# Optimization experiments

Measured on AMD Instinct MI355X. Metric: run time of the kernel, lower is better.

## Reference

```python
import jax, jax.numpy as jnp
import numpy as np
import math

B, T, C = 2, 8192, 1024
H = 16
HD = C // H  # 64
WIN = 256    # local_window_size


def _rope_tables(T, hd):
    inv_freq = 1.0 / (10000.0 ** (np.arange(0, hd, 2, dtype=np.float32) / hd))
    t = np.arange(T, dtype=np.float32)
    freqs = np.outer(t, inv_freq)                      # [T, hd/2]
    emb = np.concatenate([freqs, freqs], axis=-1)      # [T, hd]
    return jnp.asarray(np.cos(emb))[None, None], jnp.asarray(np.sin(emb))[None, None]


def setup_inputs() -> dict:
    key = jax.random.key(0)
    ks = jax.random.split(key, 10)
    x = jax.random.normal(ks[0], (B, T, C), dtype=jnp.float32)
    # padding_mask: bool [B,T]; per the source, True positions end up masked out of attention
    padding_mask = jax.random.randint(ks[1], (B, T), 0, 2).astype(bool)
    cos, sin = _rope_tables(T, HD)                     # [1,1,T,HD]
    s = 1.0 / math.sqrt(C)
    Wq = jax.random.normal(ks[2], (C, C), dtype=jnp.float32) * s
    bq = jnp.zeros((C,), dtype=jnp.float32)
    Wk = jax.random.normal(ks[3], (C, C), dtype=jnp.float32) * s
    bk = jnp.zeros((C,), dtype=jnp.float32)
    Wv = jax.random.normal(ks[4], (C, C), dtype=jnp.float32) * s
    bv = jnp.zeros((C,), dtype=jnp.float32)
    Wo = jax.random.normal(ks[5], (C, C), dtype=jnp.float32) * s
    bo = jnp.zeros((C,), dtype=jnp.float32)
    return {"x": x, "padding_mask": padding_mask, "cos": cos, "sin": sin,
            "Wq": Wq, "bq": bq, "Wk": Wk, "bk": bk, "Wv": Wv, "bv": bv,
            "Wo": Wo, "bo": bo}


def _rotate_half(t):
    h = t.shape[-1] // 2
    return jnp.concatenate([-t[..., h:], t[..., :h]], axis=-1)


def reference(x, padding_mask, cos, sin, Wq, bq, Wk, bk, Wv, bv, Wo, bo):
    Bx, Tx, Cx = x.shape
    Wn = WIN
    pad_end = (Wn - Tx % Wn) % Wn            # static python int
    Tp = Tx + pad_end
    nW = Tp // Wn
    half = Wn // 2
    hd = cos.shape[-1]

    cos_t = jnp.broadcast_to(cos[0, 0][None], (Bx, Tx, hd))
    sin_t = jnp.broadcast_to(sin[0, 0][None], (Bx, Tx, hd))
    if pad_end > 0:
        x = jnp.pad(x, ((0, 0), (0, pad_end), (0, 0)))
        padding_mask = jnp.pad(padding_mask, ((0, 0), (0, pad_end)))
        cos_t = jnp.pad(cos_t, ((0, 0), (0, pad_end), (0, 0)))
        sin_t = jnp.pad(sin_t, ((0, 0), (0, pad_end), (0, 0)))

    # non-overlapping query windows: [B*nW, W, C]
    q_win = x.reshape(Bx * nW, Wn, Cx)
    cos_q = cos_t.reshape(Bx * nW, Wn, hd)[:, None]   # [Bw,1,W,hd]
    sin_q = sin_t.reshape(Bx * nW, Wn, hd)[:, None]

    # overlapping key/value windows of size 2W, stride W
    x_ctx = jnp.pad(x, ((0, 0), (half, half), (0, 0)))
    cos_ctx = jnp.pad(cos_t, ((0, 0), (half, half), (0, 0)))
    sin_ctx = jnp.pad(sin_t, ((0, 0), (half, half), (0, 0)))
    pk = jnp.pad(padding_mask, ((0, 0), (half, half)))  # pad value False
    idx = jnp.arange(nW)[:, None] * Wn + jnp.arange(2 * Wn)[None, :]  # [nW, 2W]
    k_win = x_ctx[:, idx].reshape(Bx * nW, 2 * Wn, Cx)
    cos_k = cos_ctx[:, idx].reshape(Bx * nW, 2 * Wn, hd)[:, None]
    sin_k = sin_ctx[:, idx].reshape(Bx * nW, 2 * Wn, hd)[:, None]
    pk = pk[:, idx].reshape(Bx * nW, 2 * Wn)

    # attn_mask: True = attend (SDPA bool-mask convention)
    attn_mask = ~pk
    all_attend = jnp.all(attn_mask, axis=-1)
    attn_mask = attn_mask.at[:, 0].set(jnp.where(all_attend, False, attn_mask[:, 0]))

    Bw = Bx * nW
    q = (q_win @ Wq.T + bq).reshape(Bw, Wn, H, HD).transpose(0, 2, 1, 3)        # [Bw,H,W,hd]
    k = (k_win @ Wk.T + bk).reshape(Bw, 2 * Wn, H, HD).transpose(0, 2, 1, 3)    # [Bw,H,2W,hd]
    v = (k_win @ Wv.T + bv).reshape(Bw, 2 * Wn, H, HD).transpose(0, 2, 1, 3)

    q = q * cos_q + _rotate_half(q) * sin_q
    k = k * cos_k + _rotate_half(k) * sin_k

    scale = 1.0 / math.sqrt(HD)
    scores = jnp.einsum('bhqd,bhkd->bhqk', q, k) * scale                        # [Bw,H,W,2W]
    scores = jnp.where(attn_mask[:, None, None, :], scores, jnp.finfo(scores.dtype).min)
    attn = jax.nn.softmax(scores, axis=-1)
    out = jnp.einsum('bhqk,bhkd->bhqd', attn, v)
    out = out.transpose(0, 2, 1, 3).reshape(Bw, Wn, Cx)
    out = out @ Wo.T + bo
    out = out.reshape(Bx, nW * Wn, Cx)[:, :Tx]
    return out
```

## Files before the change

kernel.cpp:

```cpp
#include <hip/hip_runtime.h>
#include <hip/hip_bf16.h>
#include <stdint.h>

#define T_SEQ 8192
#define B_SZ 2
#define CDIM 1024
#define NH 16
#define HDIM 64
#define NW 32

typedef unsigned short ushort_t;
typedef __attribute__((ext_vector_type(8))) short short8;
typedef __attribute__((ext_vector_type(8))) unsigned short us8;
typedef __attribute__((ext_vector_type(4))) unsigned short us4;
typedef __attribute__((ext_vector_type(4))) float f32x4;

__device__ __forceinline__ unsigned short f2bf(float f) {
  union { float f; unsigned int u; } c; c.f = f;
  return (unsigned short)((c.u + 0x7FFFu + ((c.u >> 16) & 1u)) >> 16);
}
__device__ __forceinline__ unsigned pk2(float a, float b) {
  unsigned r;
  asm("v_cvt_pk_bf16_f32 %0, %1, %2" : "=v"(r) : "v"(a), "v"(b));
  return r;
}
__device__ __forceinline__ void gld16(void* lds, const void* g) {
  __builtin_amdgcn_global_load_lds(
      (const __attribute__((address_space(1))) void*)g,
      (__attribute__((address_space(3))) void*)lds, 16, 0, 0);
}

__global__ __launch_bounds__(256) void cvt_f32_bf16(const float* __restrict__ src,
                                                    ushort_t* __restrict__ dst, int n4)
{
  int i = blockIdx.x * 256 + threadIdx.x;
  if (i < n4) {
    float4 v = ((const float4*)src)[i];
    ushort4 o;
    o.x = f2bf(v.x); o.y = f2bf(v.y); o.z = f2bf(v.z); o.w = f2bf(v.w);
    ((ushort4*)dst)[i] = o;
  }
}

__global__ __launch_bounds__(256) void cvt_w4(const float* __restrict__ w0,
                                              const float* __restrict__ w1,
                                              const float* __restrict__ w2,
                                              const float* __restrict__ w3,
                                              ushort_t* __restrict__ dst)
{
  const float* srcs[4] = {w0, w1, w2, w3};
  const float* s = srcs[blockIdx.y];
  ushort_t* d = dst + (size_t)blockIdx.y * CDIM * CDIM;
  int i = blockIdx.x * 256 + threadIdx.x;
  float4 v = ((const float4*)s)[i];
  ushort4 o;
  o.x = f2bf(v.x); o.y = f2bf(v.y); o.z = f2bf(v.z); o.w = f2bf(v.w);
  ((ushort4*)d)[i] = o;
}

__device__ __forceinline__ void gemm256_core(const ushort_t* __restrict__ A,
                                             const ushort_t* __restrict__ W,
                                             ushort_t* SH,
                                             int m0, int n0, int t, f32x4 acc[8][4])
{
  const int lane = t & 63;
  const int wv = t >> 6;
  const int wr = wv >> 2;
  const int wc = wv & 3;
  const int fr = lane & 15;
  const int quad = lane >> 4;

  ushort_t* As = SH;
  ushort_t* Bs = SH + 32768;

  const int sr8 = lane >> 3;
  const int scb = ((lane & 7) ^ sr8) * 8;
  const int srowb = wv * 8 + sr8;
  const ushort_t* Ag = A + (size_t)(m0 + srowb) * CDIM + scb;
  const ushort_t* Wg = W + (size_t)(n0 + srowb) * CDIM + scb;
  ushort_t* lA = As + srowb * 64 + (lane & 7) * 8;
  ushort_t* lB = Bs + srowb * 64 + (lane & 7) * 8;

#pragma unroll
  for (int p = 0; p < 4; p++) {
    gld16(lA + p * 4096, Ag + (size_t)p * 64 * CDIM);
    gld16(lB + p * 4096, Wg + (size_t)p * 64 * CDIM);
  }
  __syncthreads();

  for (int kt = 0; kt < CDIM / 64; ++kt) {
    const int cur = kt & 1;
    if (kt + 1 < CDIM / 64) {
      const ushort_t* Agn = Ag + (kt + 1) * 64;
      const ushort_t* Wgn = Wg + (kt + 1) * 64;
      ushort_t* nA = lA + (cur ^ 1) * 16384;
      ushort_t* nB = lB + (cur ^ 1) * 16384;
#pragma unroll
      for (int p = 0; p < 4; p++) {
        gld16(nA + p * 4096, Agn + (size_t)p * 64 * CDIM);
        gld16(nB + p * 4096, Wgn + (size_t)p * 64 * CDIM);
      }
    }
    const ushort_t* Ac = As + cur * 16384;
    const ushort_t* Bc = Bs + cur * 16384;
    short8 b[4][2];
#pragma unroll
    for (int j = 0; j < 4; j++)
#pragma unroll
      for (int ks = 0; ks < 2; ks++)
        b[j][ks] = *(const short8*)&Bc[(wc * 64 + j * 16 + fr) * 64 +
                                       (((ks * 4 + quad) ^ (fr & 7)) * 8)];
    __builtin_amdgcn_s_setprio(1);
#pragma unroll
    for (int i = 0; i < 8; i++) {
      const int ra = (wr * 128 + i * 16 + fr) * 64;
      short8 a0 = *(const short8*)&Ac[ra + ((quad ^ (fr & 7)) * 8)];
      short8 a1 = *(const short8*)&Ac[ra + (((4 + quad) ^ (fr & 7)) * 8)];
#pragma unroll
      for (int j = 0; j < 4; j++)
        acc[i][j] = __builtin_amdgcn_mfma_f32_16x16x32_bf16(a0, b[j][0], acc[i][j], 0, 0, 0);
#pragma unroll
      for (int j = 0; j < 4; j++)
        acc[i][j] = __builtin_amdgcn_mfma_f32_16x16x32_bf16(a1, b[j][1], acc[i][j], 0, 0, 0);
    }
    __builtin_amdgcn_s_setprio(0);
    __syncthreads();
  }
}

__device__ __forceinline__ void xcd_swz(int& bx, int& by) {
  int gx = gridDim.x, nwg = gx * gridDim.y;
  int lid = bx + gx * by;
  int cpx = nwg >> 3;
  int swz = (lid & 7) * cpx + (lid >> 3);
  bx = swz % gx;
  by = swz / gx;
}

__global__ __launch_bounds__(512, 1) void gemm_qkv(const ushort_t* __restrict__ A,
                                                   const ushort_t* __restrict__ Wcat,
                                                   const float* __restrict__ bq,
                                                   const float* __restrict__ bk,
                                                   const float* __restrict__ bv,
                                                   ushort_t* __restrict__ Qb,
                                                   ushort_t* __restrict__ Kb,
                                                   ushort_t* __restrict__ Vtb,
                                                   const float* __restrict__ cosT,
                                                   const float* __restrict__ sinT)
{
  extern __shared__ ushort_t SH[];

  const int t = threadIdx.x;
  const int lane = t & 63;
  const int wv = t >> 6;
  const int wr = wv >> 2;
  const int wc = wv & 3;
  const int fr = lane & 15;
  const int quad = lane >> 4;
  int bx = blockIdx.x, by = blockIdx.y;
  xcd_swz(bx, by);
  const int m0 = by * 256;
  const int n0 = bx * 256;
  const int sec = bx >> 2;
  const int nsec0 = (bx & 3) * 256;
  const float* bias = (sec == 0) ? bq : (sec == 1) ? bk : bv;

  f32x4 acc[8][4];
#pragma unroll
  for (int i = 0; i < 8; i++)
#pragma unroll
    for (int j = 0; j < 4; j++) acc[i][j] = (f32x4){0.f, 0.f, 0.f, 0.f};

  gemm256_core(A, Wcat, SH, m0, n0, t, acc);

  if (sec < 2) {
    ushort_t* OutQK = sec ? Kb : Qb;
#pragma unroll
    for (int half = 0; half < 2; ++half) {
      if (wr == half) {
#pragma unroll
        for (int jp = 0; jp < 2; jp++) {
          int d = jp * 16 + fr;
          int cl = wc * 64 + jp * 16 + fr;
          float bl = bias[nsec0 + cl];
          float bh = bias[nsec0 + cl + 32];
#pragma unroll
          for (int i = 0; i < 8; i++) {
            int rloc = i * 16 + quad * 4;
#pragma unroll
            for (int r = 0; r < 4; r++) {
              int m = m0 + half * 128 + rloc + r;
              int tt = m & (T_SEQ - 1);
              float c = cosT[tt * HDIM + d];
              float sn = sinT[tt * HDIM + d];
              float lo = acc[i][jp][r] + bl;
              float hi = acc[i][jp + 2][r] + bh;
              SH[(rloc + r) * 264 + cl] = f2bf(lo * c - hi * sn);
              SH[(rloc + r) * 264 + cl + 32] = f2bf(hi * c + lo * sn);
            }
          }
        }
      }
      __syncthreads();
      const int rr0 = t >> 5;
      const int c8 = (t & 31) * 8;
      size_t gbase = (size_t)(m0 + half * 128) * CDIM + nsec0 + c8;
#pragma unroll
      for (int pp = 0; pp < 8; pp++) {
        int rr = pp * 16 + rr0;
        *(us8*)&OutQK[gbase + (size_t)rr * CDIM] = *(const us8*)&SH[rr * 264 + c8];
      }
      __syncthreads();
    }
  } else {
#pragma unroll
    for (int j = 0; j < 4; j++) {
      int ch = nsec0 + wc * 64 + j * 16 + fr;
      float bvv = bias[ch];
#pragma unroll
      for (int i = 0; i < 8; i++) {
        int m = m0 + wr * 128 + i * 16 + quad * 4;
        int bb = m >> 13;
        int tq = m & (T_SEQ - 1);
        us4 pk;
#pragma unroll
        for (int r = 0; r < 4; r++) pk[r] = f2bf(acc[i][j][r] + bvv);
        *(us4*)&Vtb[((size_t)bb * CDIM + ch) * T_SEQ + tq] = pk;
      }
    }
  }
}

__global__ __launch_bounds__(512, 1) void gemm_out(const ushort_t* __restrict__ A,
                                                   const ushort_t* __restrict__ W,
                                                   const float* __restrict__ bias,
                                                   float* __restrict__ Out)
{
  extern __shared__ ushort_t SH[];

  const int t = threadIdx.x;
  const int lane = t & 63;
  const int wv = t >> 6;
  const int wr = wv >> 2;
  const int wc = wv & 3;
  const int fr = lane & 15;
  const int quad = lane >> 4;
  int bx = blockIdx.x, by = blockIdx.y;
  xcd_swz(bx, by);
  const int m0 = by * 256;
  const int n0 = bx * 256;

  f32x4 acc[8][4];
#pragma unroll
  for (int i = 0; i < 8; i++)
#pragma unroll
    for (int j = 0; j < 4; j++) acc[i][j] = (f32x4){0.f, 0.f, 0.f, 0.f};

  gemm256_core(A, W, SH, m0, n0, t, acc);

#pragma unroll
  for (int j = 0; j < 4; j++) {
    int n = n0 + wc * 64 + j * 16 + fr;
    float bvv = bias[n];
#pragma unroll
    for (int i = 0; i < 8; i++) {
      int m = m0 + wr * 128 + i * 16 + quad * 4;
#pragma unroll
      for (int r = 0; r < 4; r++)
        Out[(size_t)(m + r) * CDIM + n] = acc[i][j][r] + bvv;
    }
  }
}

__global__ __launch_bounds__(256, 4) void attn_kernel(const ushort_t* __restrict__ Q,
                                                      const ushort_t* __restrict__ Kg,
                                                      const ushort_t* __restrict__ Vt,
                                                      const int* __restrict__ mask,
                                                      ushort_t* __restrict__ AO)
{
  __shared__ ushort_t Ks[64 * 72];
  __shared__ ushort_t Vts[64 * 72];
  __shared__ unsigned int PsW[4 * 32 * 32];
  __shared__ float attf[512];

  const int t = threadIdx.x;
  const int lane = t & 63;
  const int wv = t >> 6;
  const int h = blockIdx.x;
  const int w = blockIdx.y >> 1;
  const int qh = blockIdx.y & 1;
  const int b = blockIdx.z;
  const int fr = lane & 15;
  const int quad = lane >> 4;

  {
    int p0 = w * 256 + t - 128;
    bool a0 = (p0 < 0 || p0 >= T_SEQ) ? true : (mask[b * T_SEQ + p0] == 0);
    int p1 = p0 + 256;
    bool a1 = (p1 < 0 || p1 >= T_SEQ) ? true : (mask[b * T_SEQ + p1] == 0);
    int all1 = __syncthreads_and((int)(a0 && a1));
    attf[t] = a0 ? 0.f : -1.0e38f;
    attf[t + 256] = a1 ? 0.f : -1.0e38f;
    if (all1 && t == 0) attf[0] = -1.0e38f;
  }

  short8 qf[2][2];
  {
    const ushort_t* qp = Q + ((size_t)b * T_SEQ + w * 256 + qh * 128 + wv * 32 + fr) * CDIM
                           + h * HDIM + quad * 8;
#pragma unroll
    for (int mt = 0; mt < 2; mt++)
#pragma unroll
      for (int ks = 0; ks < 2; ks++)
        qf[mt][ks] = *(const short8*)&qp[(size_t)mt * 16 * CDIM + ks * 32];
  }

  const int srow = t >> 3;
  const int sc8 = (t & 7) * 8;
  const ushort_t* kgb = Kg + (size_t)b * T_SEQ * CDIM + h * HDIM + sc8;
  const ushort_t* vt_base = Vt + ((size_t)b * CDIM + h * HDIM) * T_SEQ;
  const float SCL = 0.18033688011112042f;

  unsigned int* pw = &PsW[wv * 1024];
  const int swz = (fr & 7) << 2;
  const int rbase = quad << 2;

  float m_run[2], l_run[2];
  f32x4 o[2][4];
#pragma unroll
  for (int mt = 0; mt < 2; mt++) { m_run[mt] = -3.0e38f; l_run[mt] = 0.f; }
#pragma unroll
  for (int mt = 0; mt < 2; mt++)
#pragma unroll
    for (int nt = 0; nt < 4; nt++) o[mt][nt] = (f32x4){0.f, 0.f, 0.f, 0.f};

  for (int kc = 0; kc < 8; kc++) {
    __syncthreads();
    {
#pragma unroll
      for (int p = 0; p < 2; p++) {
        int jj = p * 32 + srow;
        int pos = w * 256 + kc * 64 + jj - 128;
        us8 kval = (us8)(0);
        if (pos >= 0 && pos < T_SEQ) kval = *(const us8*)&kgb[(size_t)pos * CDIM];
        *(us8*)&Ks[jj * 72 + sc8] = kval;
      }
      int pos0 = w * 256 + kc * 64 - 128 + sc8;
      bool inr = (pos0 >= 0) && (pos0 < T_SEQ);
#pragma unroll
      for (int p = 0; p < 2; p++) {
        int d = p * 32 + srow;
        us8 vv = (us8)(0);
        if (inr) vv = *(const us8*)&vt_base[(size_t)d * T_SEQ + pos0];
        *(us8*)&Vts[d * 72 + sc8] = vv;
      }
    }
    __syncthreads();

    short8 kf[4][2];
#pragma unroll
    for (int nt = 0; nt < 4; nt++)
#pragma unroll
      for (int ks = 0; ks < 2; ks++)
        kf[nt][ks] = *(const short8*)&Ks[(nt * 16 + fr) * 72 + ks * 32 + quad * 8];

    f32x4 st[2][4];
    __builtin_amdgcn_s_setprio(1);
#pragma unroll
    for (int mt = 0; mt < 2; mt++)
#pragma unroll
      for (int nt = 0; nt < 4; nt++) {
        f32x4 a = (f32x4){0.f, 0.f, 0.f, 0.f};
        a = __builtin_amdgcn_mfma_f32_16x16x32_bf16(kf[nt][0], qf[mt][0], a, 0, 0, 0);
        a = __builtin_amdgcn_mfma_f32_16x16x32_bf16(kf[nt][1], qf[mt][1], a, 0, 0, 0);
        st[mt][nt] = a;
      }
    __builtin_amdgcn_s_setprio(0);

    f32x4 kb[4];
#pragma unroll
    for (int nt = 0; nt < 4; nt++)
      kb[nt] = *(const f32x4*)&attf[kc * 64 + nt * 16 + quad * 4];
#pragma unroll
    for (int mt = 0; mt < 2; mt++)
#pragma unroll
      for (int nt = 0; nt < 4; nt++)
#pragma unroll
        for (int r = 0; r < 4; r++)
          st[mt][nt][r] = __builtin_fmaf(st[mt][nt][r], SCL, kb[nt][r]);

#pragma unroll
    for (int mt = 0; mt < 2; mt++) {
      float t0 = fmaxf(fmaxf(st[mt][0][0], st[mt][0][1]), fmaxf(st[mt][0][2], st[mt][0][3]));
      float t1 = fmaxf(fmaxf(st[mt][1][0], st[mt][1][1]), fmaxf(st[mt][1][2], st[mt][1][3]));
      float t2 = fmaxf(fmaxf(st[mt][2][0], st[mt][2][1]), fmaxf(st[mt][2][2], st[mt][2][3]));
      float t3 = fmaxf(fmaxf(st[mt][3][0], st[mt][3][1]), fmaxf(st[mt][3][2], st[mt][3][3]));
      float mx = fmaxf(fmaxf(t0, t1), fmaxf(t2, t3));
      mx = fmaxf(mx, __shfl_xor(mx, 16, 64));
      mx = fmaxf(mx, __shfl_xor(mx, 32, 64));
      if (!__all(mx <= m_run[mt] + 8.f)) {
        float mnew = fmaxf(m_run[mt], mx);
        float alpha = __builtin_amdgcn_exp2f(m_run[mt] - mnew);
        m_run[mt] = mnew;
        l_run[mt] *= alpha;
        float af[4];
#pragma unroll
        for (int r = 0; r < 4; r++) af[r] = __shfl(alpha, rbase + r, 64);
#pragma unroll
        for (int nt = 0; nt < 4; nt++)
#pragma unroll
          for (int r = 0; r < 4; r++) o[mt][nt][r] *= af[r];
      }
      float rs = 0.f;
#pragma unroll
      for (int nt = 0; nt < 4; nt++)
#pragma unroll
        for (int r = 0; r < 4; r++) {
          float p = __builtin_amdgcn_exp2f(st[mt][nt][r] - m_run[mt]);
          st[mt][nt][r] = p;
          rs += p;
        }
      rs += __shfl_xor(rs, 16, 64);
      rs += __shfl_xor(rs, 32, 64);
      l_run[mt] += rs;

      unsigned int* pr = pw + ((mt * 16 + fr) << 5);
#pragma unroll
      for (int nt = 0; nt < 4; nt++)
#pragma unroll
        for (int hh = 0; hh < 2; hh++)
          pr[(((nt << 3) + (quad << 1) + hh)) ^ swz] =
              pk2(st[mt][nt][2 * hh], st[mt][nt][2 * hh + 1]);
    }

    short8 vf[4][2];
#pragma unroll
    for (int nt = 0; nt < 4; nt++)
#pragma unroll
      for (int ks = 0; ks < 2; ks++)
        vf[nt][ks] = *(const short8*)&Vts[(nt * 16 + fr) * 72 + ks * 32 + quad * 8];

    __builtin_amdgcn_s_setprio(1);
#pragma unroll
    for (int mt = 0; mt < 2; mt++) {
      const unsigned int* pr = pw + ((mt * 16 + fr) << 5);
      short8 pf[2];
#pragma unroll
      for (int ks = 0; ks < 2; ks++)
        pf[ks] = *(const short8*)&pr[((ks << 4) + (quad << 2)) ^ swz];
#pragma unroll
      for (int nt = 0; nt < 4; nt++) {
        o[mt][nt] = __builtin_amdgcn_mfma_f32_16x16x32_bf16(pf[0], vf[nt][0], o[mt][nt], 0, 0, 0);
        o[mt][nt] = __builtin_amdgcn_mfma_f32_16x16x32_bf16(pf[1], vf[nt][1], o[mt][nt], 0, 0, 0);
      }
    }
    __builtin_amdgcn_s_setprio(0);
  }

  size_t obase = ((size_t)b * T_SEQ + w * 256 + qh * 128 + wv * 32) * CDIM + h * HDIM;
#pragma unroll
  for (int mt = 0; mt < 2; mt++)
#pragma unroll
    for (int r = 0; r < 4; r++) {
      float lv = __shfl(l_run[mt], rbase + r, 64);
      float iv = 1.0f / fmaxf(lv, 1e-30f);
      int row = mt * 16 + quad * 4 + r;
#pragma unroll
      for (int nt = 0; nt < 4; nt++)
        AO[obase + (size_t)row * CDIM + nt * 16 + fr] = f2bf(o[mt][nt][r] * iv);
    }
}

extern "C" void kernel_launch(void* const* d_in, const int* in_sizes, int n_in,
                              void* d_out, int out_size, void* d_ws, size_t ws_size,
                              hipStream_t stream)
{
  const float* x    = (const float*)d_in[0];
  const int*   pm   = (const int*)d_in[1];
  const float* cosT = (const float*)d_in[2];
  const float* sinT = (const float*)d_in[3];
  const float* Wq   = (const float*)d_in[4];
  const float* bq   = (const float*)d_in[5];
  const float* Wk   = (const float*)d_in[6];
  const float* bk   = (const float*)d_in[7];
  const float* Wv   = (const float*)d_in[8];
  const float* bv   = (const float*)d_in[9];
  const float* Wo   = (const float*)d_in[10];
  const float* bo   = (const float*)d_in[11];
  float* out = (float*)d_out;

  static bool attr_done = false;
  if (!attr_done) {
    hipFuncSetAttribute(reinterpret_cast<const void*>(gemm_qkv),
                        hipFuncAttributeMaxDynamicSharedMemorySize, 131072);
    hipFuncSetAttribute(reinterpret_cast<const void*>(gemm_out),
                        hipFuncAttributeMaxDynamicSharedMemorySize, 131072);
    attr_done = true;
  }

  const size_t NTOK = (size_t)B_SZ * T_SEQ;
  const size_t NELT = NTOK * CDIM;
  ushort_t* Kb  = (ushort_t*)d_out;
  ushort_t* xbf = (ushort_t*)d_out + NELT;
  char* ws = (char*)d_ws;
  ushort_t* Wbf = (ushort_t*)ws;
  ushort_t* Qb  = (ushort_t*)(ws + 4 * (size_t)CDIM * CDIM * 2);
  ushort_t* Vtb = Qb + NELT;
  ushort_t* AO  = Qb;

  cvt_f32_bf16<<<(int)(NELT / 4 / 256), 256, 0, stream>>>(x, xbf, (int)(NELT / 4));
  cvt_w4<<<dim3(CDIM * CDIM / 4 / 256, 4), 256, 0, stream>>>(Wq, Wk, Wv, Wo, Wbf);

  gemm_qkv<<<dim3(12, (int)(NTOK / 256)), 512, 131072, stream>>>(
      xbf, Wbf, bq, bk, bv, Qb, Kb, Vtb, cosT, sinT);

  attn_kernel<<<dim3(NH, NW * 2, B_SZ), 256, 0, stream>>>(Qb, Kb, Vtb, pm, AO);

  gemm_out<<<dim3(4, (int)(NTOK / 256)), 512, 131072, stream>>>(
      AO, Wbf + 3 * (size_t)CDIM * CDIM, bo, out);
}
```

Baseline: 406.8 us.

## Halve GEMM K-tile to 32 and allow two workgroups per CU

The shared GEMM core now stages 32-wide K slices instead of 64, using a 4-way XOR swizzle, which halves LDS per workgroup (64KB double-buffered). Launch bounds change from 1 to 2 blocks per CU so two 512-thread workgroups can co-reside and hide latency. The cost is twice as many K iterations with a barrier each, and a tighter register budget (acc[8][4] per thread) that may cause spills.

```diff
diff --git a/kernel.cpp b/kernel.cpp
--- a/kernel.cpp
+++ b/kernel.cpp
@@ -71,57 +71,49 @@
   const int quad = lane >> 4;
 
   ushort_t* As = SH;
-  ushort_t* Bs = SH + 32768;
-
-  const int sr8 = lane >> 3;
-  const int scb = ((lane & 7) ^ sr8) * 8;
-  const int srowb = wv * 8 + sr8;
-  const ushort_t* Ag = A + (size_t)(m0 + srowb) * CDIM + scb;
-  const ushort_t* Wg = W + (size_t)(n0 + srowb) * CDIM + scb;
-  ushort_t* lA = As + srowb * 64 + (lane & 7) * 8;
-  ushort_t* lB = Bs + srowb * 64 + (lane & 7) * 8;
-
-#pragma unroll
-  for (int p = 0; p < 4; p++) {
-    gld16(lA + p * 4096, Ag + (size_t)p * 64 * CDIM);
-    gld16(lB + p * 4096, Wg + (size_t)p * 64 * CDIM);
+  ushort_t* Bs = SH + 16384;
+
+  const int r0 = wv * 16 + (lane >> 2);
+  const int scb = ((lane & 3) ^ (r0 & 3)) * 8;
+  const ushort_t* Ag = A + (size_t)(m0 + r0) * CDIM + scb;
+  const ushort_t* Wg = W + (size_t)(n0 + r0) * CDIM + scb;
+  ushort_t* lA = As + r0 * 32 + (lane & 3) * 8;
+  ushort_t* lB = Bs + r0 * 32 + (lane & 3) * 8;
+
+#pragma unroll
+  for (int p = 0; p < 2; p++) {
+    gld16(lA + p * 4096, Ag + (size_t)p * 128 * CDIM);
+    gld16(lB + p * 4096, Wg + (size_t)p * 128 * CDIM);
   }
   __syncthreads();
 
-  for (int kt = 0; kt < CDIM / 64; ++kt) {
+  const int rblk = (quad ^ (fr & 3)) * 8;
+
+  for (int kt = 0; kt < CDIM / 32; ++kt) {
     const int cur = kt & 1;
-    if (kt + 1 < CDIM / 64) {
-      const ushort_t* Agn = Ag + (kt + 1) * 64;
-      const ushort_t* Wgn = Wg + (kt + 1) * 64;
-      ushort_t* nA = lA + (cur ^ 1) * 16384;
-      ushort_t* nB = lB + (cur ^ 1) * 16384;
-#pragma unroll
-      for (int p = 0; p < 4; p++) {
-        gld16(nA + p * 4096, Agn + (size_t)p * 64 * CDIM);
-        gld16(nB + p * 4096, Wgn + (size_t)p * 64 * CDIM);
-      }
-    }
-    const ushort_t* Ac = As + cur * 16384;
-    const ushort_t* Bc = Bs + cur * 16384;
-    short8 b[4][2];
+    if (kt + 1 < CDIM / 32) {
+      const int kc = (kt + 1) * 32;
+      ushort_t* nA = lA + (cur ^ 1) * 8192;
+      ushort_t* nB = lB + (cur ^ 1) * 8192;
+#pragma unroll
+      for (int p = 0; p < 2; p++) {
+        gld16(nA + p * 4096, Ag + (size_t)p * 128 * CDIM + kc);
+        gld16(nB + p * 4096, Wg + (size_t)p * 128 * CDIM + kc);
+      }
+    }
+    const ushort_t* Ac = As + cur * 8192;
+    const ushort_t* Bc = Bs + cur * 8192;
+    short8 b[4];
 #pragma unroll
     for (int j = 0; j < 4; j++)
-#pragma unroll
-      for (int ks = 0; ks < 2; ks++)
-        b[j][ks] = *(const short8*)&Bc[(wc * 64 + j * 16 + fr) * 64 +
-                                       (((ks * 4 + quad) ^ (fr & 7)) * 8)];
+      b[j] = *(const short8*)&Bc[(wc * 64 + j * 16 + fr) * 32 + rblk];
     __builtin_amdgcn_s_setprio(1);
 #pragma unroll
     for (int i = 0; i < 8; i++) {
-      const int ra = (wr * 128 + i * 16 + fr) * 64;
-      short8 a0 = *(const short8*)&Ac[ra + ((quad ^ (fr & 7)) * 8)];
-      short8 a1 = *(const short8*)&Ac[ra + (((4 + quad) ^ (fr & 7)) * 8)];
+      short8 a = *(const short8*)&Ac[(wr * 128 + i * 16 + fr) * 32 + rblk];
 #pragma unroll
       for (int j = 0; j < 4; j++)
-        acc[i][j] = __builtin_amdgcn_mfma_f32_16x16x32_bf16(a0, b[j][0], acc[i][j], 0, 0, 0);
-#pragma unroll
-      for (int j = 0; j < 4; j++)
-        acc[i][j] = __builtin_amdgcn_mfma_f32_16x16x32_bf16(a1, b[j][1], acc[i][j], 0, 0, 0);
+        acc[i][j] = __builtin_amdgcn_mfma_f32_16x16x32_bf16(a, b[j], acc[i][j], 0, 0, 0);
     }
     __builtin_amdgcn_s_setprio(0);
     __syncthreads();
@@ -137,7 +129,7 @@
   by = swz / gx;
 }
 
-__global__ __launch_bounds__(512, 1) void gemm_qkv(const ushort_t* __restrict__ A,
+__global__ __launch_bounds__(512, 2) void gemm_qkv(const ushort_t* __restrict__ A,
                                                    const ushort_t* __restrict__ Wcat,
                                                    const float* __restrict__ bq,
                                                    const float* __restrict__ bk,
@@ -231,7 +223,7 @@
   }
 }
 
-__global__ __launch_bounds__(512, 1) void gemm_out(const ushort_t* __restrict__ A,
+__global__ __launch_bounds__(512, 2) void gemm_out(const ushort_t* __restrict__ A,
                                                    const ushort_t* __restrict__ W,
                                                    const float* __restrict__ bias,
                                                    float* __restrict__ Out)
@@ -511,11 +503,11 @@
   cvt_f32_bf16<<<(int)(NELT / 4 / 256), 256, 0, stream>>>(x, xbf, (int)(NELT / 4));
   cvt_w4<<<dim3(CDIM * CDIM / 4 / 256, 4), 256, 0, stream>>>(Wq, Wk, Wv, Wo, Wbf);
 
-  gemm_qkv<<<dim3(12, (int)(NTOK / 256)), 512, 131072, stream>>>(
+  gemm_qkv<<<dim3(12, (int)(NTOK / 256)), 512, 67584, stream>>>(
       xbf, Wbf, bq, bk, bv, Qb, Kb, Vtb, cosT, sinT);
 
   attn_kernel<<<dim3(NH, NW * 2, B_SZ), 256, 0, stream>>>(Qb, Kb, Vtb, pm, AO);
 
-  gemm_out<<<dim3(4, (int)(NTOK / 256)), 512, 131072, stream>>>(
+  gemm_out<<<dim3(4, (int)(NTOK / 256)), 512, 65536, stream>>>(
       AO, Wbf + 3 * (size_t)CDIM * CDIM, bo, out);
 }
```

New measurement: 422.8 us. 1.04x slower.
